# Kernel optimization log

Measured on AMD Instinct MI355X. Metric: run time of the kernel, lower is better.

Reference implementation:

```python
import jax, jax.numpy as jnp
import numpy as np

GROUPS = 32
EPS = 1e-6


def group_norm(x, scale, bias):
    b, c, h, w = x.shape
    xg = x.reshape(b, GROUPS, c // GROUPS, h, w)
    mean = xg.mean(axis=(2, 3, 4), keepdims=True)
    var = xg.var(axis=(2, 3, 4), keepdims=True)
    xg = (xg - mean) * jax.lax.rsqrt(var + EPS)
    x = xg.reshape(b, c, h, w)
    return x * scale[None, :, None, None] + bias[None, :, None, None]


def conv1x1(x, w, b):
    # x: [B,C,H,W], w: [O,C], b: [O]
    return jnp.einsum('bchw,oc->bohw', x, w) + b[None, :, None, None]


def setup_inputs() -> dict:
    key = jax.random.key(0)
    ks = jax.random.split(key, 11)
    B, C, H, W = 4, 512, 64, 64
    s = 1.0 / np.sqrt(C)
    return {
        'x': jax.random.normal(ks[0], (B, C, H, W), jnp.float32),
        'gn_scale': jnp.ones((C,), jnp.float32),
        'gn_bias': jnp.zeros((C,), jnp.float32),
        'wq': jax.random.normal(ks[1], (C, C), jnp.float32) * s,
        'bq': jnp.zeros((C,), jnp.float32),
        'wk': jax.random.normal(ks[2], (C, C), jnp.float32) * s,
        'bk': jnp.zeros((C,), jnp.float32),
        'wv': jax.random.normal(ks[3], (C, C), jnp.float32) * s,
        'bv': jnp.zeros((C,), jnp.float32),
        'wp': jax.random.normal(ks[4], (C, C), jnp.float32) * s,
        'bp': jnp.zeros((C,), jnp.float32),
    }


def reference(x, gn_scale, gn_bias, wq, bq, wk, bk, wv, bv, wp, bp):
    b, c, h, w = x.shape
    h_ = group_norm(x, gn_scale, gn_bias)
    q = conv1x1(h_, wq, bq).reshape(b, c, h * w)  # [B,C,N]
    k = conv1x1(h_, wk, bk).reshape(b, c, h * w)
    v = conv1x1(h_, wv, bv).reshape(b, c, h * w)
    # scores[b,i,j] = sum_c q[b,c,i]*k[b,c,j] / sqrt(c)
    scores = jnp.einsum('bci,bcj->bij', q, k) * (c ** -0.5)
    attn = jax.nn.softmax(scores, axis=2)
    # out[b,c,i] = sum_j attn[b,i,j] * v[b,c,j]
    out = jnp.einsum('bij,bcj->bci', attn, v).reshape(b, c, h, w)
    out = conv1x1(out, wp, bp)
    return x + out
```

## Files before the change

kernel.cpp:

```cpp
#include <hip/hip_runtime.h>

#define CDIM 512
#define NDIM 4096
#define BATCH 4

using bf8v = __attribute__((ext_vector_type(8))) __bf16;
using f4v  = __attribute__((ext_vector_type(4))) float;

typedef __attribute__((address_space(1))) unsigned int gu32;
typedef __attribute__((address_space(3))) unsigned int lu32;

static __device__ __forceinline__ unsigned short f2bf(float f) {
  unsigned int u = __float_as_uint(f);
  u += 0x7fffu + ((u >> 16) & 1u);
  return (unsigned short)(u >> 16);
}

static __device__ __forceinline__ bf8v lds_read16(const unsigned short* p) {
  bf8v r;
  unsigned off = (unsigned)(unsigned long long)p;
  asm volatile("ds_read_b128 %0, %1" : "=v"(r) : "v"(off));
  return r;
}

__global__ __launch_bounds__(256) void gn_stats_kernel(
    const float* __restrict__ x, float* __restrict__ stats) {
  const int tid = threadIdx.x;
  const float4* xv = (const float4*)(x + (long)blockIdx.x * 65536);
  float s = 0.f, ss = 0.f;
  for (int i = tid; i < 16384; i += 256) {
    float4 d = xv[i];
    s  += d.x + d.y + d.z + d.w;
    ss += d.x * d.x + d.y * d.y + d.z * d.z + d.w * d.w;
  }
#pragma unroll
  for (int off = 32; off; off >>= 1) {
    s  += __shfl_down(s, off);
    ss += __shfl_down(ss, off);
  }
  __shared__ float red[8];
  if ((tid & 63) == 0) { red[tid >> 6] = s; red[4 + (tid >> 6)] = ss; }
  __syncthreads();
  if (tid == 0) {
    float S  = red[0] + red[1] + red[2] + red[3];
    float SS = red[4] + red[5] + red[6] + red[7];
    float mean = S * (1.f / 65536.f);
    float var  = SS * (1.f / 65536.f) - mean * mean;
    stats[blockIdx.x * 2]     = mean;
    stats[blockIdx.x * 2 + 1] = rsqrtf(var + 1e-6f);
  }
}

__global__ __launch_bounds__(256) void gn_transpose_kernel(
    const float* __restrict__ x, const float* __restrict__ gs,
    const float* __restrict__ gb, const float* __restrict__ stats,
    unsigned short* __restrict__ hT) {
  __shared__ float t[64][65];
  const int tid = threadIdx.x;
  const int b = blockIdx.z;
  const long bbx = (long)b * ((long)CDIM * NDIM);
  const int n0 = blockIdx.x * 64, c0 = blockIdx.y * 64;
  for (int k = 0; k < 4; ++k) {
    int it = tid + k * 256;
    int c = it >> 4, no = (it & 15) << 2;
    int ch = c0 + c;
    int g = ch >> 4;
    float mean = stats[(b * 32 + g) * 2];
    float rstd = stats[(b * 32 + g) * 2 + 1];
    float a  = rstd * gs[ch];
    float bb = gb[ch] - mean * a;
    float4 d = *(const float4*)&x[bbx + (long)ch * NDIM + n0 + no];
    t[no + 0][c] = d.x * a + bb;
    t[no + 1][c] = d.y * a + bb;
    t[no + 2][c] = d.z * a + bb;
    t[no + 3][c] = d.w * a + bb;
  }
  __syncthreads();
  const long bbh = (long)b * ((long)NDIM * CDIM);
  for (int k = 0; k < 2; ++k) {
    int it = tid + k * 256;
    int n = it >> 3, co = (it & 7) << 3;
    unsigned int ow[4];
#pragma unroll
    for (int j = 0; j < 4; ++j) {
      unsigned short lo = f2bf(t[n][co + 2 * j]);
      unsigned short hi = f2bf(t[n][co + 2 * j + 1]);
      ow[j] = (unsigned int)lo | ((unsigned int)hi << 16);
    }
    uint4 o; o.x = ow[0]; o.y = ow[1]; o.z = ow[2]; o.w = ow[3];
    *(uint4*)&hT[bbh + (long)(n0 + n) * CDIM + c0 + co] = o;
  }
}

__global__ __launch_bounds__(256) void prep_kernel(
    const float* __restrict__ wq, const float* __restrict__ wk,
    const float* __restrict__ wv, const float* __restrict__ bq,
    const float* __restrict__ bk, unsigned short* __restrict__ wqkb,
    unsigned short* __restrict__ wvb, float* __restrict__ bqk) {
  int blk = blockIdx.x;
  if (blk < 768) {
    int i = blk * 256 + threadIdx.x;
    const float* src = (blk < 256) ? wq : (blk < 512) ? wk : wv;
    unsigned short* dst = (blk < 256) ? wqkb : (blk < 512) ? (wqkb + 262144) : wvb;
    int j = i - ((blk < 256) ? 0 : (blk < 512) ? 65536 : 131072);
    float4 d = ((const float4*)src)[j];
    ushort4 o;
    o.x = f2bf(d.x); o.y = f2bf(d.y); o.z = f2bf(d.z); o.w = f2bf(d.w);
    ((ushort4*)dst)[j] = o;
  } else {
#pragma unroll
    for (int k = 0; k < 4; ++k) {
      int i = threadIdx.x + k * 256;
      bqk[i] = (i < 512) ? bq[i] : bk[i - 512];
    }
  }
}

__global__ __launch_bounds__(256) void cvt_kernel(
    const float* __restrict__ src, unsigned short* __restrict__ dst, int n4) {
  int i = blockIdx.x * 256 + threadIdx.x;
  if (i >= n4) return;
  float4 d = ((const float4*)src)[i];
  ushort4 o;
  o.x = f2bf(d.x); o.y = f2bf(d.y); o.z = f2bf(d.z); o.w = f2bf(d.w);
  ((ushort4*)dst)[i] = o;
}


template <int EPI, int ORD>
__global__ __launch_bounds__(256, 2) void gemm4(
    const unsigned short* __restrict__ A, long sA, int lA,
    const unsigned short* __restrict__ B, long sB, int lB,
    void* __restrict__ Cp, long sC,
    const float* __restrict__ bias,
    const float* __restrict__ X, long sX,
    int GX, int GY, int Nn, int K) {
  constexpr int BM = 128, BN = 128;
  constexpr int TM = 4, TN = 4;
  constexpr int LA = 4, LB = 4;

  __shared__ __align__(16) unsigned short As[2 * BM * 64];
  __shared__ __align__(16) unsigned short Bs[2 * BN * 64];

  const int tid = threadIdx.x;
  const int nwg = gridDim.x;
  const int g = (blockIdx.x & 7) * (nwg >> 3) + (blockIdx.x >> 3);
  int bx, by, bz;
  if (ORD == 0) { bx = g % GX; int t = g / GX; by = t % GY; bz = t / GY; }
  else          { by = g % GY; int t = g / GY; bx = t % GX; bz = t / GX; }

  A += (long)bz * sA;
  B += (long)bz * sB;
  const int m0 = by * BM;
  const int n0 = bx * BN;
  const int lane = tid & 63;
  const int wv = tid >> 6;
  const int wm = (wv >> 1) * 64;
  const int wn = (wv & 1) * 64;
  const int l16 = lane & 15;
  const int quad = lane >> 4;
  const int sw7 = l16 & 7;
  const int rg0 = ((0 + quad) ^ sw7) << 3;
  const int rg1 = ((4 + quad) ^ sw7) << 3;

  const int r0s  = wv * 8 + (lane >> 3);
  const int gsrc = ((lane & 7) ^ (lane >> 3)) << 3;
  const unsigned short* Ag = A + (long)(m0 + r0s) * lA + gsrc;
  const unsigned short* Bg = B + (long)(n0 + r0s) * lB + gsrc;

  const int nt = K >> 6;

  auto stage = [&](int t) {
    if (t < nt) {
      const int k0 = t << 6;
      unsigned short* Ad = As + (t & 1) * (BM * 64) + wv * 512;
      unsigned short* Bd = Bs + (t & 1) * (BN * 64) + wv * 512;
#pragma unroll
      for (int i = 0; i < LA; ++i)
        __builtin_amdgcn_global_load_lds(
            (const gu32*)(Ag + (long)i * 32 * lA + k0),
            (lu32*)(Ad + i * 2048), 16, 0, 0);
#pragma unroll
      for (int i = 0; i < LB; ++i)
        __builtin_amdgcn_global_load_lds(
            (const gu32*)(Bg + (long)i * 32 * lB + k0),
            (lu32*)(Bd + i * 2048), 16, 0, 0);
    }
  };

  f4v acc[TM][TN] = {};
  f4v accr[TM] = {};
  bf8v ones;
#pragma unroll
  for (int i = 0; i < 8; ++i) ones[i] = (__bf16)1.0f;

  bf8v bfr[TN][2];
  bf8v afA[2][2], afB[2][2];

  const unsigned short* Ab;
  const unsigned short* Bb;

  auto rdB = [&]() {
#pragma unroll
    for (int tn = 0; tn < TN; ++tn) {
      bfr[tn][0] = lds_read16(&Bb[(wn + tn * 16 + l16) * 64 + rg0]);
      bfr[tn][1] = lds_read16(&Bb[(wn + tn * 16 + l16) * 64 + rg1]);
    }
  };
  auto rdA = [&](int q, bf8v (&fr)[2][2]) {
#pragma unroll
    for (int dr = 0; dr < 2; ++dr) {
      fr[dr][0] = lds_read16(&Ab[(wm + (q * 2 + dr) * 16 + l16) * 64 + rg0]);
      fr[dr][1] = lds_read16(&Ab[(wm + (q * 2 + dr) * 16 + l16) * 64 + rg1]);
    }
  };
  auto clus = [&](int q, bf8v (&fr)[2][2]) {
    __builtin_amdgcn_s_setprio(1);
#pragma unroll
    for (int kk = 0; kk < 2; ++kk)
#pragma unroll
      for (int dr = 0; dr < 2; ++dr) {
        const int tm = q * 2 + dr;
#pragma unroll
        for (int tn = 0; tn < TN; ++tn)
          acc[tm][tn] = __builtin_amdgcn_mfma_f32_16x16x32_bf16(
              fr[dr][kk], bfr[tn][kk], acc[tm][tn], 0, 0, 0);
        if (EPI == 3)
          accr[tm] = __builtin_amdgcn_mfma_f32_16x16x32_bf16(
              fr[dr][kk], ones, accr[tm], 0, 0, 0);
      }
    __builtin_amdgcn_s_setprio(0);
  };

  stage(0);
  for (int t = 0; t < nt; ++t) {
    asm volatile("s_waitcnt vmcnt(0)");
    __builtin_amdgcn_s_barrier();
    stage(t + 1);
    Ab = As + (t & 1) * (BM * 64);
    Bb = Bs + (t & 1) * (BN * 64);
    rdB();
    rdA(0, afA);
    rdA(1, afB);
    asm volatile("s_waitcnt lgkmcnt(4)");
    __builtin_amdgcn_sched_barrier(0);
    clus(0, afA);
    asm volatile("s_waitcnt lgkmcnt(0)");
    __builtin_amdgcn_sched_barrier(0);
    clus(1, afB);
  }

  if (EPI == 2) {
#pragma unroll
    for (int tm = 0; tm < TM; ++tm) {
#pragma unroll
      for (int r = 0; r < 4; ++r) {
        const int row = m0 + wm + tm * 16 + quad * 4 + r;
#pragma unroll
        for (int tn = 0; tn < TN; ++tn) {
          const int col = n0 + wn + tn * 16 + l16;
          float e = __expf(acc[tm][tn][r] * 0.044194173824159216f);
          ((unsigned short*)Cp)[(long)bz * sC + (long)row * Nn + col] = f2bf(e);
        }
      }
    }
  } else if (EPI == 3) {
#pragma unroll
    for (int tm = 0; tm < TM; ++tm) {
#pragma unroll
      for (int r = 0; r < 4; ++r) {
        const int row = m0 + wm + tm * 16 + quad * 4 + r;
        const float inv = 1.0f / accr[tm][r];
#pragma unroll
        for (int tn = 0; tn < TN; ++tn) {
          const int col = n0 + wn + tn * 16 + l16;
          ((unsigned short*)Cp)[(long)bz * sC + (long)row * Nn + col] =
              f2bf(acc[tm][tn][r] * inv);
        }
      }
    }
  } else {
#pragma unroll
    for (int tm = 0; tm < TM; ++tm) {
#pragma unroll
      for (int tn = 0; tn < TN; ++tn) {
        const int col = n0 + wn + tn * 16 + l16;
#pragma unroll
        for (int r = 0; r < 4; ++r) {
          const int row = m0 + wm + tm * 16 + quad * 4 + r;
          float val = acc[tm][tn][r];
          if (EPI == 0) {
            val += bias[col];
            ((unsigned short*)Cp)[(long)bz * sC + (long)row * Nn + col] = f2bf(val);
          } else if (EPI == 1) {
            val += bias[row];
            ((unsigned short*)Cp)[(long)bz * sC + (long)row * Nn + col] = f2bf(val);
          } else {
            ((float*)Cp)[(long)bz * sC + (long)row * Nn + col] =
                val + bias[row] + X[(long)bz * sX + (long)row * Nn + col];
          }
        }
      }
    }
  }
}

template <int EPI, int ORD>
__global__ __launch_bounds__(512, 4) void gemm8n(
    const unsigned short* __restrict__ A, long sA, int lA,
    const unsigned short* __restrict__ B, long sB, int lB,
    void* __restrict__ Cp, long sC,
    const float* __restrict__ bias,
    const float* __restrict__ X, long sX,
    int GX, int GY, int Nn, int K) {
  constexpr int BM = 256, BN = 128;
  constexpr int TM = 4, TN = 4;

  __shared__ __align__(16) unsigned short As[2 * BM * 32];
  __shared__ __align__(16) unsigned short Bs[2 * BN * 32];

  const int tid = threadIdx.x;
  const int nwg = gridDim.x;
  const int g = (blockIdx.x & 7) * (nwg >> 3) + (blockIdx.x >> 3);
  int bx, by, bz;
  if (ORD == 0) { bx = g % GX; int t = g / GX; by = t % GY; bz = t / GY; }
  else          { by = g % GY; int t = g / GY; bx = t % GX; bz = t / GX; }

  A += (long)bz * sA;
  B += (long)bz * sB;
  const int m0 = by * BM;
  const int n0 = bx * BN;
  const int lane = tid & 63;
  const int wv = tid >> 6;
  const int wm = (wv >> 1) * 64;
  const int wn = (wv & 1) * 64;
  const int l16 = lane & 15;
  const int quad = lane >> 4;
  const int rg = (quad ^ ((l16 >> 1) & 3)) << 3;

  const int rl = tid >> 2;
  const int gl = tid & 3;
  const int gsrc = (gl ^ ((rl >> 1) & 3)) << 3;
  const unsigned short* Ag = A + (long)(m0 + rl) * lA + gsrc;
  const unsigned short* Bg = B + (long)(n0 + rl) * lB + gsrc;

  const int nt = K >> 5;

  auto stage = [&](int t) {
    if (t < nt) {
      const int k0 = t << 5;
      unsigned short* Ad = As + (t & 1) * (BM * 32) + wv * 512;
      unsigned short* Bd = Bs + (t & 1) * (BN * 32) + wv * 512;
      __builtin_amdgcn_global_load_lds((const gu32*)(Ag + k0),
                                       (lu32*)(Ad), 16, 0, 0);
      __builtin_amdgcn_global_load_lds((const gu32*)(Ag + (long)128 * lA + k0),
                                       (lu32*)(Ad + 4096), 16, 0, 0);
      __builtin_amdgcn_global_load_lds((const gu32*)(Bg + k0),
                                       (lu32*)(Bd), 16, 0, 0);
    }
  };

  f4v acc[TM][TN] = {};
  f4v accr[TM] = {};
  bf8v ones;
#pragma unroll
  for (int i = 0; i < 8; ++i) ones[i] = (__bf16)1.0f;

  stage(0);
  for (int t = 0; t < nt; ++t) {
    asm volatile("s_waitcnt vmcnt(0)");
    __builtin_amdgcn_s_barrier();
    stage(t + 1);
    const unsigned short* Ab = As + (t & 1) * (BM * 32);
    const unsigned short* Bb = Bs + (t & 1) * (BN * 32);
    bf8v af[TM], bf[TN];
#pragma unroll
    for (int tn = 0; tn < TN; ++tn)
      bf[tn] = lds_read16(&Bb[(wn + tn * 16 + l16) * 32 + rg]);
#pragma unroll
    for (int tm = 0; tm < TM; ++tm)
      af[tm] = lds_read16(&Ab[(wm + tm * 16 + l16) * 32 + rg]);
    asm volatile("s_waitcnt lgkmcnt(2)");
    __builtin_amdgcn_sched_barrier(0);
    __builtin_amdgcn_s_setprio(1);
#pragma unroll
    for (int tm = 0; tm < 2; ++tm) {
#pragma unroll
      for (int tn = 0; tn < TN; ++tn)
        acc[tm][tn] = __builtin_amdgcn_mfma_f32_16x16x32_bf16(
            af[tm], bf[tn], acc[tm][tn], 0, 0, 0);
      if (EPI == 3)
        accr[tm] = __builtin_amdgcn_mfma_f32_16x16x32_bf16(
            af[tm], ones, accr[tm], 0, 0, 0);
    }
    __builtin_amdgcn_s_setprio(0);
    asm volatile("s_waitcnt lgkmcnt(0)");
    __builtin_amdgcn_sched_barrier(0);
    __builtin_amdgcn_s_setprio(1);
#pragma unroll
    for (int tm = 2; tm < TM; ++tm) {
#pragma unroll
      for (int tn = 0; tn < TN; ++tn)
        acc[tm][tn] = __builtin_amdgcn_mfma_f32_16x16x32_bf16(
            af[tm], bf[tn], acc[tm][tn], 0, 0, 0);
      if (EPI == 3)
        accr[tm] = __builtin_amdgcn_mfma_f32_16x16x32_bf16(
            af[tm], ones, accr[tm], 0, 0, 0);
    }
    __builtin_amdgcn_s_setprio(0);
  }

  if (EPI == 2) {
#pragma unroll
    for (int tm = 0; tm < TM; ++tm) {
#pragma unroll
      for (int r = 0; r < 4; ++r) {
        const int row = m0 + wm + tm * 16 + quad * 4 + r;
#pragma unroll
        for (int tn = 0; tn < TN; ++tn) {
          const int col = n0 + wn + tn * 16 + l16;
          float e = __expf(acc[tm][tn][r] * 0.044194173824159216f);
          ((unsigned short*)Cp)[(long)bz * sC + (long)row * Nn + col] = f2bf(e);
        }
      }
    }
  } else if (EPI == 3) {
#pragma unroll
    for (int tm = 0; tm < TM; ++tm) {
#pragma unroll
      for (int r = 0; r < 4; ++r) {
        const int row = m0 + wm + tm * 16 + quad * 4 + r;
        const float inv = 1.0f / accr[tm][r];
#pragma unroll
        for (int tn = 0; tn < TN; ++tn) {
          const int col = n0 + wn + tn * 16 + l16;
          ((unsigned short*)Cp)[(long)bz * sC + (long)row * Nn + col] =
              f2bf(acc[tm][tn][r] * inv);
        }
      }
    }
  } else {
#pragma unroll
    for (int tm = 0; tm < TM; ++tm) {
#pragma unroll
      for (int tn = 0; tn < TN; ++tn) {
        const int col = n0 + wn + tn * 16 + l16;
#pragma unroll
        for (int r = 0; r < 4; ++r) {
          const int row = m0 + wm + tm * 16 + quad * 4 + r;
          float val = acc[tm][tn][r];
          if (EPI == 0) {
            val += bias[col];
            ((unsigned short*)Cp)[(long)bz * sC + (long)row * Nn + col] = f2bf(val);
          } else if (EPI == 1) {
            val += bias[row];
            ((unsigned short*)Cp)[(long)bz * sC + (long)row * Nn + col] = f2bf(val);
          } else {
            ((float*)Cp)[(long)bz * sC + (long)row * Nn + col] =
                val + bias[row] + X[(long)bz * sX + (long)row * Nn + col];
          }
        }
      }
    }
  }
}

extern "C" void kernel_launch(void* const* d_in, const int* in_sizes, int n_in,
                              void* d_out, int out_size, void* d_ws, size_t ws_size,
                              hipStream_t stream) {
  (void)in_sizes; (void)n_in; (void)out_size;
  const float* x  = (const float*)d_in[0];
  const float* gs = (const float*)d_in[1];
  const float* gb = (const float*)d_in[2];
  const float* wq = (const float*)d_in[3];
  const float* bq = (const float*)d_in[4];
  const float* wk = (const float*)d_in[5];
  const float* bk = (const float*)d_in[6];
  const float* wv = (const float*)d_in[7];
  const float* bv = (const float*)d_in[8];
  const float* wp = (const float*)d_in[9];
  const float* bp = (const float*)d_in[10];
  float* out = (float*)d_out;

  char* ws = (char*)d_ws;
  const long NC  = (long)NDIM * CDIM;
  const long NQK = (long)NDIM * 1024;
  const long BUF = NC * 2 * BATCH;
  const long NN  = (long)NDIM * NDIM;

  unsigned short* hT   = (unsigned short*)(ws);
  unsigned short* OT   = hT;
  unsigned short* qkT  = (unsigned short*)(ws + BUF);
  unsigned short* vB   = (unsigned short*)(ws + BUF * 3);
  unsigned short* sc   = (unsigned short*)(ws + BUF * 4);
  unsigned short* wqkb = sc;
  unsigned short* wvb  = (unsigned short*)(ws + BUF * 4 + 1048576);
  float* bqk           = (float*)(ws + BUF * 4 + 1572864);
  float* stats         = (float*)(ws + BUF * 4 + 1581056);
  unsigned short* wpb  = qkT;

  gn_stats_kernel<<<BATCH * 32, 256, 0, stream>>>(x, stats);
  gn_transpose_kernel<<<dim3(NDIM / 64, CDIM / 64, BATCH), 256, 0, stream>>>(x, gs, gb, stats, hT);
  prep_kernel<<<769, 256, 0, stream>>>(wq, wk, wv, bq, bk, wqkb, wvb, bqk);

  gemm8n<0, 0><<<512, 512, 0, stream>>>(
      hT, NC, CDIM, wqkb, 0, CDIM, qkT, NQK, bqk, nullptr, 0, 8, 16, 1024, CDIM);
  gemm4<1, 1><<<512, 256, 0, stream>>>(
      wvb, 0, CDIM, hT, NC, CDIM, vB, NC, bv, nullptr, 0, 32, 4, NDIM, CDIM);

  if (ws_size >= (size_t)(BUF * 4) + (size_t)(NN * 2) * BATCH) {
    gemm8n<2, 0><<<2048, 512, 0, stream>>>(
        qkT, NQK, 1024, qkT + 512, NQK, 1024, sc, NN, nullptr, nullptr, 0,
        32, 16, NDIM, CDIM);
    gemm4<3, 1><<<512, 256, 0, stream>>>(
        sc, NN, NDIM, vB, NC, NDIM, OT, NC, nullptr, nullptr, 0,
        4, 32, CDIM, NDIM);
  } else {
    for (int b = 0; b < BATCH; ++b) {
      gemm8n<2, 0><<<512, 512, 0, stream>>>(
          qkT + b * NQK, 0, 1024, qkT + b * NQK + 512, 0, 1024, sc, 0,
          nullptr, nullptr, 0, 32, 16, NDIM, CDIM);
      gemm4<3, 1><<<128, 256, 0, stream>>>(
          sc, 0, NDIM, vB + b * NC, 0, NDIM, OT + b * NC, 0,
          nullptr, nullptr, 0, 4, 32, CDIM, NDIM);
    }
  }

  cvt_kernel<<<256, 256, 0, stream>>>(wp, wpb, 65536);
  gemm4<4, 1><<<512, 256, 0, stream>>>(
      wpb, 0, CDIM, OT, NC, CDIM, out, NC, bp, x, NC, 32, 4, NDIM, CDIM);
}
```

Measured before the change: 339.2 us.

## Use triple-buffered LDS pipeline with K=32 tiles in both GEMM kernels

Both GEMM kernels move from double-buffered LDS to a three-slot ring buffer. Loads are issued two k-steps ahead, and the wait only blocks on the oldest outstanding stage (vmcnt(4)/vmcnt(3)) instead of draining all loads. The 128x128 kernel also drops from K=64 to K=32 tiles and reuses the gemm8n swizzle and compute body. This aims to hide global-load latency better, at the cost of more barriers per K and a change in LDS footprint and occupancy.

```diff
diff --git a/kernel.cpp b/kernel.cpp
--- a/kernel.cpp
+++ b/kernel.cpp
@@ -128,19 +128,17 @@
 
 
 template <int EPI, int ORD>
-__global__ __launch_bounds__(256, 2) void gemm4(
+__global__ __launch_bounds__(256, 2) void gemm4n(
     const unsigned short* __restrict__ A, long sA, int lA,
     const unsigned short* __restrict__ B, long sB, int lB,
     void* __restrict__ Cp, long sC,
     const float* __restrict__ bias,
     const float* __restrict__ X, long sX,
     int GX, int GY, int Nn, int K) {
-  constexpr int BM = 128, BN = 128;
   constexpr int TM = 4, TN = 4;
-  constexpr int LA = 4, LB = 4;
-
-  __shared__ __align__(16) unsigned short As[2 * BM * 64];
-  __shared__ __align__(16) unsigned short Bs[2 * BN * 64];
+
+  __shared__ __align__(16) unsigned short As[3 * 128 * 32];
+  __shared__ __align__(16) unsigned short Bs[3 * 128 * 32];
 
   const int tid = threadIdx.x;
   const int nwg = gridDim.x;
@@ -151,40 +149,37 @@
 
   A += (long)bz * sA;
   B += (long)bz * sB;
-  const int m0 = by * BM;
-  const int n0 = bx * BN;
+  const int m0 = by * 128;
+  const int n0 = bx * 128;
   const int lane = tid & 63;
   const int wv = tid >> 6;
   const int wm = (wv >> 1) * 64;
   const int wn = (wv & 1) * 64;
   const int l16 = lane & 15;
   const int quad = lane >> 4;
-  const int sw7 = l16 & 7;
-  const int rg0 = ((0 + quad) ^ sw7) << 3;
-  const int rg1 = ((4 + quad) ^ sw7) << 3;
-
-  const int r0s  = wv * 8 + (lane >> 3);
-  const int gsrc = ((lane & 7) ^ (lane >> 3)) << 3;
-  const unsigned short* Ag = A + (long)(m0 + r0s) * lA + gsrc;
-  const unsigned short* Bg = B + (long)(n0 + r0s) * lB + gsrc;
-
-  const int nt = K >> 6;
-
-  auto stage = [&](int t) {
+  const int rg = (quad ^ ((l16 >> 1) & 3)) << 3;
+
+  const int rl = tid >> 2;
+  const int gl = tid & 3;
+  const int gsrc = (gl ^ ((rl >> 1) & 3)) << 3;
+  const unsigned short* Ag = A + (long)(m0 + rl) * lA + gsrc;
+  const unsigned short* Bg = B + (long)(n0 + rl) * lB + gsrc;
+
+  const int nt = K >> 5;
+
+  auto stage = [&](int t, int sl) {
     if (t < nt) {
-      const int k0 = t << 6;
-      unsigned short* Ad = As + (t & 1) * (BM * 64) + wv * 512;
-      unsigned short* Bd = Bs + (t & 1) * (BN * 64) + wv * 512;
-#pragma unroll
-      for (int i = 0; i < LA; ++i)
-        __builtin_amdgcn_global_load_lds(
-            (const gu32*)(Ag + (long)i * 32 * lA + k0),
-            (lu32*)(Ad + i * 2048), 16, 0, 0);
-#pragma unroll
-      for (int i = 0; i < LB; ++i)
-        __builtin_amdgcn_global_load_lds(
-            (const gu32*)(Bg + (long)i * 32 * lB + k0),
-            (lu32*)(Bd + i * 2048), 16, 0, 0);
+      const int k0 = t << 5;
+      unsigned short* Ad = As + sl * 4096 + wv * 512;
+      unsigned short* Bd = Bs + sl * 4096 + wv * 512;
+      __builtin_amdgcn_global_load_lds((const gu32*)(Ag + k0),
+                                       (lu32*)(Ad), 16, 0, 0);
+      __builtin_amdgcn_global_load_lds((const gu32*)(Ag + (long)64 * lA + k0),
+                                       (lu32*)(Ad + 2048), 16, 0, 0);
+      __builtin_amdgcn_global_load_lds((const gu32*)(Bg + k0),
+                                       (lu32*)(Bd), 16, 0, 0);
+      __builtin_amdgcn_global_load_lds((const gu32*)(Bg + (long)64 * lB + k0),
+                                       (lu32*)(Bd + 2048), 16, 0, 0);
     }
   };
 
@@ -194,61 +189,60 @@
 #pragma unroll
   for (int i = 0; i < 8; ++i) ones[i] = (__bf16)1.0f;
 
-  bf8v bfr[TN][2];
-  bf8v afA[2][2], afB[2][2];
-
-  const unsigned short* Ab;
-  const unsigned short* Bb;
-
-  auto rdB = [&]() {
-#pragma unroll
-    for (int tn = 0; tn < TN; ++tn) {
-      bfr[tn][0] = lds_read16(&Bb[(wn + tn * 16 + l16) * 64 + rg0]);
-      bfr[tn][1] = lds_read16(&Bb[(wn + tn * 16 + l16) * 64 + rg1]);
-    }
-  };
-  auto rdA = [&](int q, bf8v (&fr)[2][2]) {
-#pragma unroll
-    for (int dr = 0; dr < 2; ++dr) {
-      fr[dr][0] = lds_read16(&Ab[(wm + (q * 2 + dr) * 16 + l16) * 64 + rg0]);
-      fr[dr][1] = lds_read16(&Ab[(wm + (q * 2 + dr) * 16 + l16) * 64 + rg1]);
-    }
-  };
-  auto clus = [&](int q, bf8v (&fr)[2][2]) {
+  auto body = [&](int rs) {
+    const unsigned short* Ab = As + rs * 4096;
+    const unsigned short* Bb = Bs + rs * 4096;
+    bf8v af[TM], bf[TN];
+#pragma unroll
+    for (int tn = 0; tn < TN; ++tn)
+      bf[tn] = lds_read16(&Bb[(wn + tn * 16 + l16) * 32 + rg]);
+#pragma unroll
+    for (int tm = 0; tm < TM; ++tm)
+      af[tm] = lds_read16(&Ab[(wm + tm * 16 + l16) * 32 + rg]);
+    asm volatile("s_waitcnt lgkmcnt(2)");
+    __builtin_amdgcn_sched_barrier(0);
     __builtin_amdgcn_s_setprio(1);
 #pragma unroll
-    for (int kk = 0; kk < 2; ++kk)
-#pragma unroll
-      for (int dr = 0; dr < 2; ++dr) {
-        const int tm = q * 2 + dr;
-#pragma unroll
-        for (int tn = 0; tn < TN; ++tn)
-          acc[tm][tn] = __builtin_amdgcn_mfma_f32_16x16x32_bf16(
-              fr[dr][kk], bfr[tn][kk], acc[tm][tn], 0, 0, 0);
-        if (EPI == 3)
-          accr[tm] = __builtin_amdgcn_mfma_f32_16x16x32_bf16(
-              fr[dr][kk], ones, accr[tm], 0, 0, 0);
-      }
+    for (int tm = 0; tm < 2; ++tm) {
+#pragma unroll
+      for (int tn = 0; tn < TN; ++tn)
+        acc[tm][tn] = __builtin_amdgcn_mfma_f32_16x16x32_bf16(
+            af[tm], bf[tn], acc[tm][tn], 0, 0, 0);
+      if (EPI == 3)
+        accr[tm] = __builtin_amdgcn_mfma_f32_16x16x32_bf16(
+            af[tm], ones, accr[tm], 0, 0, 0);
+    }
+    __builtin_amdgcn_s_setprio(0);
+    asm volatile("s_waitcnt lgkmcnt(0)");
+    __builtin_amdgcn_sched_barrier(0);
+    __builtin_amdgcn_s_setprio(1);
+#pragma unroll
+    for (int tm = 2; tm < TM; ++tm) {
+#pragma unroll
+      for (int tn = 0; tn < TN; ++tn)
+        acc[tm][tn] = __builtin_amdgcn_mfma_f32_16x16x32_bf16(
+            af[tm], bf[tn], acc[tm][tn], 0, 0, 0);
+      if (EPI == 3)
+        accr[tm] = __builtin_amdgcn_mfma_f32_16x16x32_bf16(
+            af[tm], ones, accr[tm], 0, 0, 0);
+    }
     __builtin_amdgcn_s_setprio(0);
   };
 
-  stage(0);
-  for (int t = 0; t < nt; ++t) {
-    asm volatile("s_waitcnt vmcnt(0)");
+  stage(0, 0);
+  stage(1, 1);
+  int rs = 0;
+  for (int t = 0; t < nt - 1; ++t) {
+    asm volatile("s_waitcnt vmcnt(4)");
     __builtin_amdgcn_s_barrier();
-    stage(t + 1);
-    Ab = As + (t & 1) * (BM * 64);
-    Bb = Bs + (t & 1) * (BN * 64);
-    rdB();
-    rdA(0, afA);
-    rdA(1, afB);
-    asm volatile("s_waitcnt lgkmcnt(4)");
-    __builtin_amdgcn_sched_barrier(0);
-    clus(0, afA);
-    asm volatile("s_waitcnt lgkmcnt(0)");
-    __builtin_amdgcn_sched_barrier(0);
-    clus(1, afB);
-  }
+    int ss = rs + 2; if (ss >= 3) ss -= 3;
+    stage(t + 2, ss);
+    body(rs);
+    ++rs; if (rs == 3) rs = 0;
+  }
+  asm volatile("s_waitcnt vmcnt(0)");
+  __builtin_amdgcn_s_barrier();
+  body(rs);
 
   if (EPI == 2) {
 #pragma unroll
@@ -313,11 +307,10 @@
     const float* __restrict__ bias,
     const float* __restrict__ X, long sX,
     int GX, int GY, int Nn, int K) {
-  constexpr int BM = 256, BN = 128;
   constexpr int TM = 4, TN = 4;
 
-  __shared__ __align__(16) unsigned short As[2 * BM * 32];
-  __shared__ __align__(16) unsigned short Bs[2 * BN * 32];
+  __shared__ __align__(16) unsigned short As[3 * 256 * 32];
+  __shared__ __align__(16) unsigned short Bs[3 * 128 * 32];
 
   const int tid = threadIdx.x;
   const int nwg = gridDim.x;
@@ -328,8 +321,8 @@
 
   A += (long)bz * sA;
   B += (long)bz * sB;
-  const int m0 = by * BM;
-  const int n0 = bx * BN;
+  const int m0 = by * 256;
+  const int n0 = bx * 128;
   const int lane = tid & 63;
   const int wv = tid >> 6;
   const int wm = (wv >> 1) * 64;
@@ -346,11 +339,11 @@
 
   const int nt = K >> 5;
 
-  auto stage = [&](int t) {
+  auto stage = [&](int t, int sl) {
     if (t < nt) {
       const int k0 = t << 5;
-      unsigned short* Ad = As + (t & 1) * (BM * 32) + wv * 512;
-      unsigned short* Bd = Bs + (t & 1) * (BN * 32) + wv * 512;
+      unsigned short* Ad = As + sl * 8192 + wv * 512;
+      unsigned short* Bd = Bs + sl * 4096 + wv * 512;
       __builtin_amdgcn_global_load_lds((const gu32*)(Ag + k0),
                                        (lu32*)(Ad), 16, 0, 0);
       __builtin_amdgcn_global_load_lds((const gu32*)(Ag + (long)128 * lA + k0),
@@ -366,13 +359,9 @@
 #pragma unroll
   for (int i = 0; i < 8; ++i) ones[i] = (__bf16)1.0f;
 
-  stage(0);
-  for (int t = 0; t < nt; ++t) {
-    asm volatile("s_waitcnt vmcnt(0)");
-    __builtin_amdgcn_s_barrier();
-    stage(t + 1);
-    const unsigned short* Ab = As + (t & 1) * (BM * 32);
-    const unsigned short* Bb = Bs + (t & 1) * (BN * 32);
+  auto body = [&](int rs) {
+    const unsigned short* Ab = As + rs * 8192;
+    const unsigned short* Bb = Bs + rs * 4096;
     bf8v af[TM], bf[TN];
 #pragma unroll
     for (int tn = 0; tn < TN; ++tn)
@@ -408,7 +397,22 @@
             af[tm], ones, accr[tm], 0, 0, 0);
     }
     __builtin_amdgcn_s_setprio(0);
-  }
+  };
+
+  stage(0, 0);
+  stage(1, 1);
+  int rs = 0;
+  for (int t = 0; t < nt - 1; ++t) {
+    asm volatile("s_waitcnt vmcnt(3)");
+    __builtin_amdgcn_s_barrier();
+    int ss = rs + 2; if (ss >= 3) ss -= 3;
+    stage(t + 2, ss);
+    body(rs);
+    ++rs; if (rs == 3) rs = 0;
+  }
+  asm volatile("s_waitcnt vmcnt(0)");
+  __builtin_amdgcn_s_barrier();
+  body(rs);
 
   if (EPI == 2) {
 #pragma unroll
@@ -505,14 +509,14 @@
 
   gemm8n<0, 0><<<512, 512, 0, stream>>>(
       hT, NC, CDIM, wqkb, 0, CDIM, qkT, NQK, bqk, nullptr, 0, 8, 16, 1024, CDIM);
-  gemm4<1, 1><<<512, 256, 0, stream>>>(
+  gemm4n<1, 1><<<512, 256, 0, stream>>>(
       wvb, 0, CDIM, hT, NC, CDIM, vB, NC, bv, nullptr, 0, 32, 4, NDIM, CDIM);
 
   if (ws_size >= (size_t)(BUF * 4) + (size_t)(NN * 2) * BATCH) {
     gemm8n<2, 0><<<2048, 512, 0, stream>>>(
         qkT, NQK, 1024, qkT + 512, NQK, 1024, sc, NN, nullptr, nullptr, 0,
         32, 16, NDIM, CDIM);
-    gemm4<3, 1><<<512, 256, 0, stream>>>(
+    gemm4n<3, 1><<<512, 256, 0, stream>>>(
         sc, NN, NDIM, vB, NC, NDIM, OT, NC, nullptr, nullptr, 0,
         4, 32, CDIM, NDIM);
   } else {
@@ -520,13 +524,13 @@
       gemm8n<2, 0><<<512, 512, 0, stream>>>(
           qkT + b * NQK, 0, 1024, qkT + b * NQK + 512, 0, 1024, sc, 0,
           nullptr, nullptr, 0, 32, 16, NDIM, CDIM);
-      gemm4<3, 1><<<128, 256, 0, stream>>>(
+      gemm4n<3, 1><<<128, 256, 0, stream>>>(
           sc, 0, NDIM, vB + b * NC, 0, NDIM, OT + b * NC, 0,
           nullptr, nullptr, 0, 4, 32, CDIM, NDIM);
     }
   }
 
   cvt_kernel<<<256, 256, 0, stream>>>(wp, wpb, 65536);
-  gemm4<4, 1><<<512, 256, 0, stream>>>(
+  gemm4n<4, 1><<<512, 256, 0, stream>>>(
       wpb, 0, CDIM, OT, NC, CDIM, out, NC, bp, x, NC, 32, 4, NDIM, CDIM);
 }
```

New measurement: 356.2 us. 1.05x slower.
